# Optimization experiments

Measured on AMD Instinct MI355X. Metric: run time of the kernel, lower is better.

The kernel has to match this reference:

```python
import jax, jax.numpy as jnp
import numpy as np

B, S, D, H, F = 4, 1024, 2048, 16, 8192
HD = D // H  # head dim = 128
EPS = 1e-5


def layer_norm(x, w, b):
    mu = jnp.mean(x, axis=-1, keepdims=True)
    var = jnp.mean(jnp.square(x - mu), axis=-1, keepdims=True)
    return (x - mu) * jax.lax.rsqrt(var + EPS) * w + b


def setup_inputs() -> dict:
    key = jax.random.key(0)
    ks = jax.random.split(key, 12)
    s = 0.02  # realistic init scale for weights
    return {
        "x": jax.random.normal(ks[0], (B, S, D), jnp.float32),
        "attention_mask": jnp.zeros((B, 1, 1, S), jnp.float32),
        "wq": jax.random.normal(ks[1], (D, D), jnp.float32) * s,
        "bq": jax.random.normal(ks[2], (D,), jnp.float32) * s,
        "wk": jax.random.normal(ks[3], (D, D), jnp.float32) * s,
        "bk": jax.random.normal(ks[4], (D,), jnp.float32) * s,
        "wv": jax.random.normal(ks[5], (D, D), jnp.float32) * s,
        "bv": jax.random.normal(ks[6], (D,), jnp.float32) * s,
        "wo": jax.random.normal(ks[7], (D, D), jnp.float32) * s,
        "bo": jax.random.normal(ks[8], (D,), jnp.float32) * s,
        "ln1_w": jnp.ones((D,), jnp.float32),
        "ln1_b": jnp.zeros((D,), jnp.float32),
        "wi": jax.random.normal(ks[9], (F, D), jnp.float32) * s,
        "bi": jax.random.normal(ks[10], (F,), jnp.float32) * s,
        "wo2": jax.random.normal(ks[11], (D, F), jnp.float32) * s,
        "bo2": jnp.zeros((D,), jnp.float32),
        "ln2_w": jnp.ones((D,), jnp.float32),
        "ln2_b": jnp.zeros((D,), jnp.float32),
    }


def reference(x, attention_mask, wq, bq, wk, bk, wv, bv, wo, bo,
              ln1_w, ln1_b, wi, bi, wo2, bo2, ln2_w, ln2_b):
    # --- self attention ---
    q = (jnp.einsum('bsd,ed->bse', x, wq) + bq).reshape(B, S, H, HD).transpose(0, 2, 1, 3)
    k = (jnp.einsum('bsd,ed->bse', x, wk) + bk).reshape(B, S, H, HD).transpose(0, 2, 1, 3)
    v = (jnp.einsum('bsd,ed->bse', x, wv) + bv).reshape(B, S, H, HD).transpose(0, 2, 1, 3)
    scores = jnp.einsum('bhqd,bhkd->bhqk', q, k) / jnp.sqrt(jnp.float32(HD))
    scores = scores + attention_mask  # additive mask, broadcast over heads/query
    probs = jax.nn.softmax(scores, axis=-1)
    ctx = jnp.einsum('bhqk,bhkd->bhqd', probs, v)
    ctx = ctx.transpose(0, 2, 1, 3).reshape(B, S, D)
    # --- attention output: dense + bias + residual + LayerNorm ---
    attn_out = layer_norm(jnp.einsum('bsd,ed->bse', ctx, wo) + bo + x, ln1_w, ln1_b)
    # --- FFN: intermediate dense + bias, GELU, output dense + bias + residual + LN ---
    inter = jnp.einsum('bsd,fd->bsf', attn_out, wi) + bi
    h = jax.nn.gelu(inter, approximate=False)
    out = layer_norm(jnp.einsum('bsf,df->bsd', h, wo2) + bo2 + attn_out, ln2_w, ln2_b)
    return out
```

## Files before the change

### kernel.cpp

```cpp
#include <hip/hip_runtime.h>
#include <hip/hip_bf16.h>
#include <cstdint>
#include <cstddef>

typedef __attribute__((ext_vector_type(8))) short short8;
typedef __attribute__((ext_vector_type(4))) float f32x4;

#define DEV static __device__ __forceinline__

constexpr int kS = 1024, kD = 2048, kH = 16, kHD = 128, kF = 8192;
constexpr int kM = 4096;
constexpr float kEPS = 1e-5f;

constexpr size_t SZ_DD   = (size_t)kD * kD * 2;
constexpr size_t SZ_FD   = (size_t)kF * kD * 2;
constexpr size_t SZ_MD16 = (size_t)kM * kD * 2;
constexpr size_t SZ_MD32 = (size_t)kM * kD * 4;
constexpr size_t OFF_WQ  = 0;
constexpr size_t OFF_WK  = OFF_WQ + SZ_DD;
constexpr size_t OFF_WV  = OFF_WK + SZ_DD;
constexpr size_t OFF_WO  = OFF_WV + SZ_DD;
constexpr size_t OFF_WI  = OFF_WO + SZ_DD;
constexpr size_t OFF_WO2 = OFF_WI + SZ_FD;
constexpr size_t OFF_XB  = OFF_WO2 + SZ_FD;
constexpr size_t OFF_Q   = OFF_XB + SZ_MD16;
constexpr size_t OFF_K   = OFF_Q + SZ_MD16;
constexpr size_t OFF_V   = OFF_K + SZ_MD16;
constexpr size_t OFF_H   = OFF_XB;
constexpr size_t OFF_CTX = OFF_V + SZ_MD16;
constexpr size_t OFF_Y1  = OFF_CTX + SZ_MD16;
constexpr size_t OFF_A1B = OFF_Y1 + SZ_MD32;
constexpr size_t OFF_Y2  = OFF_A1B + SZ_MD16;
constexpr size_t WS_NEED = OFF_Y2 + SZ_MD32;

DEV void gload16(const void* g, void* l) {
  __builtin_amdgcn_global_load_lds(
      (const __attribute__((address_space(1))) unsigned int*)g,
      (__attribute__((address_space(3))) unsigned int*)l, 16, 0, 0);
}

__global__ void cvt_bf16(const float* __restrict__ in, __hip_bfloat16* __restrict__ out, int n4) {
  int stride = gridDim.x * blockDim.x;
  for (int i = blockIdx.x * blockDim.x + threadIdx.x; i < n4; i += stride) {
    float4 v = reinterpret_cast<const float4*>(in)[i];
    union { ushort4 u; __hip_bfloat16 h[4]; } o;
    o.h[0] = __float2bfloat16(v.x);
    o.h[1] = __float2bfloat16(v.y);
    o.h[2] = __float2bfloat16(v.z);
    o.h[3] = __float2bfloat16(v.w);
    reinterpret_cast<ushort4*>(out)[i] = o.u;
  }
}

template <int MODE>
__global__ __launch_bounds__(512, 2)
void gemm256(const __hip_bfloat16* __restrict__ A,
             const __hip_bfloat16* __restrict__ Bt,
             const float* __restrict__ bias,
             float* __restrict__ out0, float* __restrict__ out1,
             void* __restrict__ outb,
             int M, int N, int K, int kLen) {
  __shared__ __align__(16) char lds[131072];
  const int tid = threadIdx.x;
  const int lane = tid & 63, w = tid >> 6;
  const int wm = w >> 2, wn = w & 3;
  const int lg = lane >> 4, lr = lane & 15;
  const int gy = M >> 8, gx = N >> 8;
  const int nwg = gridDim.x, orig = blockIdx.x;
  const int l = (orig & 7) * (nwg >> 3) + (orig >> 3);
  const int tilesPer = gx * gy;
  const int spl = l / tilesPer;
  const int rem = l - spl * tilesPer;
  const int bx = rem / gy, by = rem - bx * gy;
  const int m0 = by * 256, n0 = bx * 256;
  const int k0 = spl * kLen;
  const int NT = kLen >> 6;

  const char* gs[8];
  #pragma unroll
  for (int h = 0; h < 4; ++h) {
    const __hip_bfloat16* src = (h < 2) ? A : Bt;
    const int r0 = ((h < 2) ? m0 : n0) + (h & 1) * 128;
    #pragma unroll
    for (int i = 0; i < 2; ++i) {
      int c = i * 512 + tid;
      int row = c >> 3, slot = c & 7;
      gs[h * 2 + i] =
          (const char*)(src + (size_t)(r0 + row) * K + k0 + (slot ^ (row & 7)) * 8);
    }
  }

#define STAGE(P, H, TOFF)                                                          \
  {                                                                                \
    char* dstb = lds + (((H) < 2) ? 0 : 65536) + (P) * 32768 + ((H) & 1) * 16384;  \
    gload16(gs[(H) * 2 + 0] + (TOFF) * 128, dstb + (0 * 512 + tid) * 16);          \
    gload16(gs[(H) * 2 + 1] + (TOFF) * 128, dstb + (1 * 512 + tid) * 16);          \
  }

  auto ldA = [&](int P, int qm, int mr, int kk) {
    int row = qm * 128 + wm * 64 + mr * 16 + lr;
    return *reinterpret_cast<const short8*>(
        lds + P * 32768 + row * 128 + (((kk * 4 + lg) ^ (row & 7)) * 16));
  };
  auto ldB = [&](int P, int qn, int nr, int kk) {
    int row = qn * 128 + wn * 32 + nr * 16 + lr;
    return *reinterpret_cast<const short8*>(
        lds + 65536 + P * 32768 + row * 128 + (((kk * 4 + lg) ^ (row & 7)) * 16));
  };

  f32x4 acc[4][4][2] = {};

#define MFMA_HALF(q, kk, B)                                                     \
  _Pragma("unroll")                                                             \
  for (int mi = 0; mi < 4; ++mi)                                                \
    _Pragma("unroll")                                                           \
    for (int ni = 0; ni < 2; ++ni)                                              \
      acc[q][mi][ni] = __builtin_amdgcn_mfma_f32_16x16x32_bf16(                 \
          av[kk][mi], B[kk][ni], acc[q][mi][ni], 0, 0, 0);

#define WAIT_LGKM(n)                                                            \
  asm volatile("s_waitcnt lgkmcnt(" #n ")" ::: "memory");                       \
  __builtin_amdgcn_sched_barrier(0);

#define TILE_BODY(P, PF)                                                        \
  {                                                                             \
               \
    asm volatile("s_waitcnt vmcnt(2)" ::: "memory");                            \
    __builtin_amdgcn_s_barrier();                                               \
         \
    _Pragma("unroll")                                                           \
    for (int i = 0; i < 4; ++i) av[0][i] = ldA(P, 0, i, 0);                     \
    _Pragma("unroll")                                                           \
    for (int i = 0; i < 2; ++i) b0[0][i] = ldB(P, 0, i, 0);                     \
    _Pragma("unroll")                                                           \
    for (int i = 0; i < 4; ++i) av[1][i] = ldA(P, 0, i, 1);                     \
    _Pragma("unroll")                                                           \
    for (int i = 0; i < 2; ++i) b0[1][i] = ldB(P, 0, i, 1);                     \
    _Pragma("unroll")                                                           \
    for (int i = 0; i < 2; ++i) b1[0][i] = ldB(P, 1, i, 0);                     \
    _Pragma("unroll")                                                           \
    for (int i = 0; i < 2; ++i) b1[1][i] = ldB(P, 1, i, 1);                     \
    if (PF) STAGE((P) ^ 1, 0, 1 + (P))                                          \
    WAIT_LGKM(10)                                                               \
    __builtin_amdgcn_s_setprio(1);                                              \
    MFMA_HALF(0, 0, b0)                                                         \
    WAIT_LGKM(4)                                                                \
    MFMA_HALF(0, 1, b0)                                                         \
    __builtin_amdgcn_s_setprio(0);                                              \
    if (PF) STAGE((P) ^ 1, 2, 1 + (P))                                          \
    WAIT_LGKM(2)                                                                \
    __builtin_amdgcn_s_setprio(1);                                              \
    MFMA_HALF(1, 0, b1)                                                         \
    WAIT_LGKM(0)                                                                \
    MFMA_HALF(1, 1, b1)                                                         \
    __builtin_amdgcn_s_setprio(0);                                              \
           \
    if (PF) { asm volatile("s_waitcnt vmcnt(4)" ::: "memory"); }                \
    else    { asm volatile("s_waitcnt vmcnt(0)" ::: "memory"); }                \
    __builtin_amdgcn_s_barrier();                                               \
    _Pragma("unroll")                                                           \
    for (int i = 0; i < 4; ++i) av[0][i] = ldA(P, 1, i, 0);                     \
    _Pragma("unroll")                                                           \
    for (int i = 0; i < 4; ++i) av[1][i] = ldA(P, 1, i, 1);                     \
    if (PF) STAGE((P) ^ 1, 3, 1 + (P))                                          \
    WAIT_LGKM(4)                                                                \
    __builtin_amdgcn_s_setprio(1);                                              \
    MFMA_HALF(2, 0, b1)                                                         \
    WAIT_LGKM(0)                                                                \
    MFMA_HALF(2, 1, b1)                                                         \
    __builtin_amdgcn_s_setprio(0);                                              \
    _Pragma("unroll")                                                           \
    for (int i = 0; i < 2; ++i) b0[0][i] = ldB(P, 0, i, 0);                     \
    _Pragma("unroll")                                                           \
    for (int i = 0; i < 2; ++i) b0[1][i] = ldB(P, 0, i, 1);                     \
    if (PF) STAGE((P) ^ 1, 1, 1 + (P))                                          \
    WAIT_LGKM(2)                                                                \
    __builtin_amdgcn_s_setprio(1);                                              \
    MFMA_HALF(3, 0, b0)                                                         \
    WAIT_LGKM(0)                                                                \
    MFMA_HALF(3, 1, b0)                                                         \
    __builtin_amdgcn_s_setprio(0);                                              \
  }

  STAGE(0, 0, 0) STAGE(0, 2, 0) STAGE(0, 3, 0) STAGE(0, 1, 0)

  for (int t2 = 0; t2 < NT; t2 += 2) {
    short8 av[2][4], b0[2][2], b1[2][2];
    TILE_BODY(0, true)
    TILE_BODY(1, (t2 + 2 < NT))
    #pragma unroll
    for (int j = 0; j < 8; ++j) gs[j] += 256;
  }
#undef TILE_BODY
#undef MFMA_HALF
#undef WAIT_LGKM
#undef STAGE

  #pragma unroll
  for (int q = 0; q < 4; ++q) {
    const int qm = (q >= 2) ? 1 : 0;
    const int qn = (q == 1 || q == 2) ? 1 : 0;
    #pragma unroll
    for (int ni = 0; ni < 2; ++ni) {
      int col = n0 + qn * 128 + wn * 32 + ni * 16 + lr;
      float bvv = 0.f;
      if constexpr (MODE != 3) bvv = bias[col];
      #pragma unroll
      for (int mi = 0; mi < 4; ++mi) {
        int row0 = m0 + qm * 128 + wm * 64 + mi * 16 + lg * 4;
        #pragma unroll
        for (int r = 0; r < 4; ++r) {
          int row = row0 + r;
          float val = acc[q][mi][ni][r] + bvv;
          if constexpr (MODE == 0) {
            int which = col >> 11;
            int d = col & 2047;
            int hh = d >> 7, hd = d & 127;
            int bb = row >> 10, ss = row & 1023;
            __hip_bfloat16* base = (__hip_bfloat16*)outb + (size_t)which * ((size_t)kM * kD);
            if (which < 2)
              base[(((size_t)(bb * kH + hh)) * kS + ss) * kHD + hd] = __float2bfloat16(val);
            else
              base[(((size_t)(bb * kH + hh)) * kHD + hd) * kS + ss] = __float2bfloat16(val);
          } else if constexpr (MODE == 2) {
            float g = 0.5f * val * (1.0f + erff(val * 0.70710678118654752f));
            ((__hip_bfloat16*)outb)[(size_t)row * N + col] = __float2bfloat16(g);
          } else {
            float* o = spl ? out1 : out0;
            o[(size_t)row * N + col] = val;
          }
        }
      }
    }
  }
}

__global__ __launch_bounds__(512, 4)
void attn_fwd(const __hip_bfloat16* __restrict__ q,
              const __hip_bfloat16* __restrict__ k,
              const __hip_bfloat16* __restrict__ vt,
              const float* __restrict__ mask,
              __hip_bfloat16* __restrict__ ctx) {
  __shared__ __align__(16) char Ks[2][64 * 256];
  __shared__ __align__(16) char Vt[2][128 * 128];
  __shared__ __align__(16) char Ps[8][2048];
  const int tid = threadIdx.x, lane = tid & 63, w = tid >> 6;
  const int lg = lane >> 4, lr = lane & 15;
  const int orig = blockIdx.x;
  const int l = (orig & 7) * 64 + (orig >> 3);
  const int qt = l & 7, bh = l >> 3;
  const int b = bh >> 4;

  short8 qf[4];
  {
    const __hip_bfloat16* qp =
        q + ((size_t)bh * kS + qt * 128 + w * 16 + lr) * kHD + lg * 8;
    #pragma unroll
    for (int kk = 0; kk < 4; ++kk) qf[kk] = *reinterpret_cast<const short8*>(qp + kk * 32);
  }

  auto stage = [&](int bufi, int t) {
    #pragma unroll
    for (int i = 0; i < 2; ++i) {
      int c = i * 512 + tid;
      int row = c >> 4, slot = c & 15;
      gload16(k + ((size_t)bh * kS + t * 64 + row) * kHD + (slot ^ (row & 15)) * 8,
              Ks[bufi] + c * 16);
    }
    #pragma unroll
    for (int i = 0; i < 2; ++i) {
      int c = i * 512 + tid;
      int row = c >> 3, slot = c & 7;
      gload16(vt + ((size_t)bh * kHD + row) * kS + t * 64 + (slot ^ (row & 7)) * 8,
              Vt[bufi] + c * 16);
    }
  };

  f32x4 o[8] = {};
  float mrun[4], lrun[4];
  #pragma unroll
  for (int r = 0; r < 4; ++r) { mrun[r] = -1e30f; lrun[r] = 0.f; }
  const float scale = 0.08838834764831845f;

  stage(0, 0);
  __syncthreads();

  int buf = 0;
  for (int t = 0; t < 16; ++t) {
    if (t + 1 < 16) stage(buf ^ 1, t + 1);

    f32x4 sacc[4] = {};
    #pragma unroll
    for (int j = 0; j < 4; ++j) {
      int key = j * 16 + lr;
      #pragma unroll
      for (int kk = 0; kk < 4; ++kk) {
        short8 bfrag = *reinterpret_cast<const short8*>(
            Ks[buf] + key * 256 + (((kk * 4 + lg) ^ (key & 15)) * 16));
        sacc[j] = __builtin_amdgcn_mfma_f32_16x16x32_bf16(qf[kk], bfrag, sacc[j], 0, 0, 0);
      }
    }
    float sarr[4][4];
    #pragma unroll
    for (int j = 0; j < 4; ++j) {
      float mv = mask[(size_t)b * kS + t * 64 + j * 16 + lr];
      #pragma unroll
      for (int r = 0; r < 4; ++r) sarr[j][r] = sacc[j][r] * scale + mv;
    }
    #pragma unroll
    for (int r = 0; r < 4; ++r) {
      float tm = fmaxf(fmaxf(sarr[0][r], sarr[1][r]), fmaxf(sarr[2][r], sarr[3][r]));
      #pragma unroll
      for (int d = 1; d < 16; d <<= 1) tm = fmaxf(tm, __shfl_xor(tm, d));
      float mnew = fmaxf(mrun[r], tm);
      float alpha = __expf(mrun[r] - mnew);
      mrun[r] = mnew;
      float rs = 0.f;
      #pragma unroll
      for (int j = 0; j < 4; ++j) {
        float p = __expf(sarr[j][r] - mnew);
        sarr[j][r] = p;
        rs += p;
      }
      #pragma unroll
      for (int d = 1; d < 16; d <<= 1) rs += __shfl_xor(rs, d);
      lrun[r] = lrun[r] * alpha + rs;
      #pragma unroll
      for (int n = 0; n < 8; ++n) o[n][r] *= alpha;
    }
    #pragma unroll
    for (int r = 0; r < 4; ++r) {
      int qr = lg * 4 + r;
      #pragma unroll
      for (int j = 0; j < 4; ++j)
        *reinterpret_cast<__hip_bfloat16*>(
            Ps[w] + ((qr * 128 + (j * 16 + lr) * 2) ^ ((qr & 7) << 4))) =
            __float2bfloat16(sarr[j][r]);
    }
    #pragma unroll
    for (int kk2 = 0; kk2 < 2; ++kk2) {
      short8 pa = *reinterpret_cast<const short8*>(
          Ps[w] + ((lr * 128 + kk2 * 64 + lg * 16) ^ ((lr & 7) << 4)));
      #pragma unroll
      for (int n = 0; n < 8; ++n) {
        int hd = n * 16 + lr;
        short8 vb = *reinterpret_cast<const short8*>(
            Vt[buf] + hd * 128 + (((kk2 * 4 + lg) ^ (hd & 7)) * 16));
        o[n] = __builtin_amdgcn_mfma_f32_16x16x32_bf16(pa, vb, o[n], 0, 0, 0);
      }
    }
    __syncthreads();
    buf ^= 1;
  }

  const int h = bh & 15;
  #pragma unroll
  for (int r = 0; r < 4; ++r) {
    float inv = 1.0f / lrun[r];
    int srow = qt * 128 + w * 16 + lg * 4 + r;
    __hip_bfloat16* cp = ctx + ((size_t)b * kS + srow) * kD + h * 128 + lr;
    #pragma unroll
    for (int n = 0; n < 8; ++n) cp[n * 16] = __float2bfloat16(o[n][r] * inv);
  }
}

template <bool WB16>
__global__ void ln_fuse(const float* __restrict__ p0, const float* __restrict__ p1,
                        const float* __restrict__ bias, const float* __restrict__ res,
                        const float* __restrict__ w, const float* __restrict__ b,
                        float* __restrict__ outf, __hip_bfloat16* __restrict__ outb) {
  const int row = blockIdx.x, tid = threadIdx.x;
  const size_t base = (size_t)row * kD;
  float v[8];
  #pragma unroll
  for (int i = 0; i < 2; ++i) {
    int c4 = tid * 2 + i;
    float4 a  = reinterpret_cast<const float4*>(p0 + base)[c4];
    float4 bb = reinterpret_cast<const float4*>(p1 + base)[c4];
    float4 rr = reinterpret_cast<const float4*>(res + base)[c4];
    float4 bs = reinterpret_cast<const float4*>(bias)[c4];
    v[i * 4 + 0] = a.x + bb.x + rr.x + bs.x;
    v[i * 4 + 1] = a.y + bb.y + rr.y + bs.y;
    v[i * 4 + 2] = a.z + bb.z + rr.z + bs.z;
    v[i * 4 + 3] = a.w + bb.w + rr.w + bs.w;
  }
  float s = 0.f;
  #pragma unroll
  for (int i = 0; i < 8; ++i) s += v[i];
  #pragma unroll
  for (int off = 32; off > 0; off >>= 1) s += __shfl_down(s, off);
  __shared__ float r1[4], r2[4];
  if ((tid & 63) == 0) r1[tid >> 6] = s;
  __syncthreads();
  float mean = (r1[0] + r1[1] + r1[2] + r1[3]) * (1.0f / kD);
  float qv = 0.f;
  #pragma unroll
  for (int i = 0; i < 8; ++i) { float d = v[i] - mean; qv += d * d; }
  #pragma unroll
  for (int off = 32; off > 0; off >>= 1) qv += __shfl_down(qv, off);
  if ((tid & 63) == 0) r2[tid >> 6] = qv;
  __syncthreads();
  float rstd = rsqrtf((r2[0] + r2[1] + r2[2] + r2[3]) * (1.0f / kD) + kEPS);
  #pragma unroll
  for (int i = 0; i < 8; ++i) {
    int col = tid * 8 + i;
    float ov = (v[i] - mean) * rstd * w[col] + b[col];
    outf[base + col] = ov;
    if constexpr (WB16) outb[base + col] = __float2bfloat16(ov);
  }
}

extern "C" void kernel_launch(void* const* d_in, const int* in_sizes, int n_in,
                              void* d_out, int out_size, void* d_ws, size_t ws_size,
                              hipStream_t stream) {
  (void)in_sizes; (void)n_in; (void)out_size;
  if (ws_size < WS_NEED) return;
  const float* x    = (const float*)d_in[0];
  const float* mask = (const float*)d_in[1];
  const float* wq   = (const float*)d_in[2];
  const float* bq   = (const float*)d_in[3];
  const float* wk   = (const float*)d_in[4];
  const float* bk   = (const float*)d_in[5];
  const float* wv   = (const float*)d_in[6];
  const float* bv   = (const float*)d_in[7];
  const float* wo   = (const float*)d_in[8];
  const float* bo   = (const float*)d_in[9];
  const float* l1w  = (const float*)d_in[10];
  const float* l1b  = (const float*)d_in[11];
  const float* wi   = (const float*)d_in[12];
  const float* bi   = (const float*)d_in[13];
  const float* wo2  = (const float*)d_in[14];
  const float* bo2  = (const float*)d_in[15];
  const float* l2w  = (const float*)d_in[16];
  const float* l2b  = (const float*)d_in[17];

  char* ws = (char*)d_ws;
  __hip_bfloat16* wqb  = (__hip_bfloat16*)(ws + OFF_WQ);
  __hip_bfloat16* wkb  = (__hip_bfloat16*)(ws + OFF_WK);
  __hip_bfloat16* wvb  = (__hip_bfloat16*)(ws + OFF_WV);
  __hip_bfloat16* wob  = (__hip_bfloat16*)(ws + OFF_WO);
  __hip_bfloat16* wib  = (__hip_bfloat16*)(ws + OFF_WI);
  __hip_bfloat16* wo2b = (__hip_bfloat16*)(ws + OFF_WO2);
  __hip_bfloat16* xb   = (__hip_bfloat16*)(ws + OFF_XB);
  __hip_bfloat16* qb   = (__hip_bfloat16*)(ws + OFF_Q);
  __hip_bfloat16* kb2  = (__hip_bfloat16*)(ws + OFF_K);
  __hip_bfloat16* vtb  = (__hip_bfloat16*)(ws + OFF_V);
  __hip_bfloat16* hb   = (__hip_bfloat16*)(ws + OFF_H);
  __hip_bfloat16* ctxb = (__hip_bfloat16*)(ws + OFF_CTX);
  __hip_bfloat16* a1b  = (__hip_bfloat16*)(ws + OFF_A1B);
  float* y1   = (float*)(ws + OFF_Y1);
  float* y2   = (float*)(ws + OFF_Y2);
  float* f2p  = (float*)(ws + OFF_WQ);
  float* bqkv = (float*)(ws + OFF_Y2);

  cvt_bf16<<<2048, 256, 0, stream>>>(x,   xb,   kM * kD / 4);
  cvt_bf16<<<1024, 256, 0, stream>>>(wq,  wqb,  kD * kD / 4);
  cvt_bf16<<<1024, 256, 0, stream>>>(wk,  wkb,  kD * kD / 4);
  cvt_bf16<<<1024, 256, 0, stream>>>(wv,  wvb,  kD * kD / 4);
  cvt_bf16<<<1024, 256, 0, stream>>>(wo,  wob,  kD * kD / 4);
  cvt_bf16<<<2048, 256, 0, stream>>>(wi,  wib,  kF * kD / 4);
  cvt_bf16<<<2048, 256, 0, stream>>>(wo2, wo2b, kF * kD / 4);
  hipMemcpyAsync(bqkv,          bq, kD * 4, hipMemcpyDeviceToDevice, stream);
  hipMemcpyAsync(bqkv + kD,     bk, kD * 4, hipMemcpyDeviceToDevice, stream);
  hipMemcpyAsync(bqkv + 2 * kD, bv, kD * 4, hipMemcpyDeviceToDevice, stream);

  dim3 blk(512);
  gemm256<0><<<dim3(384), blk, 0, stream>>>(
      xb, wqb, bqkv, nullptr, nullptr, qb, kM, 6144, kD, kD);
  attn_fwd<<<dim3(512), dim3(512), 0, stream>>>(qb, kb2, vtb, mask, ctxb);
  gemm256<3><<<dim3(256), blk, 0, stream>>>(
      ctxb, wob, nullptr, y1, y2, nullptr, kM, kD, kD, kD / 2);
  ln_fuse<true><<<kM, 256, 0, stream>>>(y1, y2, bo, x, l1w, l1b, y1, a1b);
  gemm256<2><<<dim3(512), blk, 0, stream>>>(
      a1b, wib, bi, nullptr, nullptr, hb, kM, kF, kD, kD);
  gemm256<3><<<dim3(256), blk, 0, stream>>>(
      hb, wo2b, nullptr, y2, f2p, nullptr, kM, kD, kF, kF / 2);
  ln_fuse<false><<<kM, 256, 0, stream>>>(y2, f2p, bo2, y1, l2w, l2b, (float*)d_out, nullptr);
}
```

Measured before the change: 675.3 us.

## Restructure GEMM tile loop into barrier-bracketed per-quadrant phases

```diff
diff --git a/kernel.cpp b/kernel.cpp
--- a/kernel.cpp
+++ b/kernel.cpp
@@ -110,24 +110,31 @@
 
   f32x4 acc[4][4][2] = {};
 
-#define MFMA_HALF(q, kk, B)                                                     \
+#define MFMA_QUAD(q, B)                                                         \
   _Pragma("unroll")                                                             \
-  for (int mi = 0; mi < 4; ++mi)                                                \
-    _Pragma("unroll")                                                           \
-    for (int ni = 0; ni < 2; ++ni)                                              \
-      acc[q][mi][ni] = __builtin_amdgcn_mfma_f32_16x16x32_bf16(                 \
-          av[kk][mi], B[kk][ni], acc[q][mi][ni], 0, 0, 0);
-
-#define WAIT_LGKM(n)                                                            \
-  asm volatile("s_waitcnt lgkmcnt(" #n ")" ::: "memory");                       \
-  __builtin_amdgcn_sched_barrier(0);
+  for (int kk = 0; kk < 2; ++kk)                                                \
+    _Pragma("unroll")                                                           \
+    for (int mi = 0; mi < 4; ++mi)                                              \
+      _Pragma("unroll")                                                         \
+      for (int ni = 0; ni < 2; ++ni)                                            \
+        acc[q][mi][ni] = __builtin_amdgcn_mfma_f32_16x16x32_bf16(               \
+            av[kk][mi], B[kk][ni], acc[q][mi][ni], 0, 0, 0);
+
+#define PHASE_CORE(Q, B, WAITSTMT)                                              \
+    __builtin_amdgcn_s_barrier();                                               \
+    asm volatile("s_waitcnt lgkmcnt(0)" ::: "memory");                          \
+    __builtin_amdgcn_sched_barrier(0);                                          \
+    __builtin_amdgcn_s_setprio(1);                                              \
+    MFMA_QUAD(Q, B)                                                             \
+    __builtin_amdgcn_s_setprio(0);                                              \
+    WAITSTMT                                                                    \
+    __builtin_amdgcn_s_barrier();
+
+#define VM(n) asm volatile("s_waitcnt vmcnt(" #n ")" ::: "memory");
 
 #define TILE_BODY(P, PF)                                                        \
   {                                                                             \
-               \
-    asm volatile("s_waitcnt vmcnt(2)" ::: "memory");                            \
-    __builtin_amdgcn_s_barrier();                                               \
-         \
+              \
     _Pragma("unroll")                                                           \
     for (int i = 0; i < 4; ++i) av[0][i] = ldA(P, 0, i, 0);                     \
     _Pragma("unroll")                                                           \
@@ -136,53 +143,34 @@
     for (int i = 0; i < 4; ++i) av[1][i] = ldA(P, 0, i, 1);                     \
     _Pragma("unroll")                                                           \
     for (int i = 0; i < 2; ++i) b0[1][i] = ldB(P, 0, i, 1);                     \
+    if (PF) STAGE((P) ^ 1, 0, 1 + (P))                                          \
+    if (PF) { PHASE_CORE(0, b0, VM(4)) } else { PHASE_CORE(0, b0, VM(2)) }      \
+      \
     _Pragma("unroll")                                                           \
     for (int i = 0; i < 2; ++i) b1[0][i] = ldB(P, 1, i, 0);                     \
     _Pragma("unroll")                                                           \
     for (int i = 0; i < 2; ++i) b1[1][i] = ldB(P, 1, i, 1);                     \
-    if (PF) STAGE((P) ^ 1, 0, 1 + (P))                                          \
-    WAIT_LGKM(10)                                                               \
-    __builtin_amdgcn_s_setprio(1);                                              \
-    MFMA_HALF(0, 0, b0)                                                         \
-    WAIT_LGKM(4)                                                                \
-    MFMA_HALF(0, 1, b0)                                                         \
-    __builtin_amdgcn_s_setprio(0);                                              \
     if (PF) STAGE((P) ^ 1, 2, 1 + (P))                                          \
-    WAIT_LGKM(2)                                                                \
-    __builtin_amdgcn_s_setprio(1);                                              \
-    MFMA_HALF(1, 0, b1)                                                         \
-    WAIT_LGKM(0)                                                                \
-    MFMA_HALF(1, 1, b1)                                                         \
-    __builtin_amdgcn_s_setprio(0);                                              \
-           \
-    if (PF) { asm volatile("s_waitcnt vmcnt(4)" ::: "memory"); }                \
-    else    { asm volatile("s_waitcnt vmcnt(0)" ::: "memory"); }                \
-    __builtin_amdgcn_s_barrier();                                               \
+    if (PF) { PHASE_CORE(1, b1, VM(4)) } else { PHASE_CORE(1, b1, VM(0)) }      \
+                         \
     _Pragma("unroll")                                                           \
     for (int i = 0; i < 4; ++i) av[0][i] = ldA(P, 1, i, 0);                     \
     _Pragma("unroll")                                                           \
     for (int i = 0; i < 4; ++i) av[1][i] = ldA(P, 1, i, 1);                     \
     if (PF) STAGE((P) ^ 1, 3, 1 + (P))                                          \
-    WAIT_LGKM(4)                                                                \
-    __builtin_amdgcn_s_setprio(1);                                              \
-    MFMA_HALF(2, 0, b1)                                                         \
-    WAIT_LGKM(0)                                                                \
-    MFMA_HALF(2, 1, b1)                                                         \
-    __builtin_amdgcn_s_setprio(0);                                              \
+    PHASE_CORE(2, b1, )                                                         \
+      \
     _Pragma("unroll")                                                           \
     for (int i = 0; i < 2; ++i) b0[0][i] = ldB(P, 0, i, 0);                     \
     _Pragma("unroll")                                                           \
     for (int i = 0; i < 2; ++i) b0[1][i] = ldB(P, 0, i, 1);                     \
     if (PF) STAGE((P) ^ 1, 1, 1 + (P))                                          \
-    WAIT_LGKM(2)                                                                \
-    __builtin_amdgcn_s_setprio(1);                                              \
-    MFMA_HALF(3, 0, b0)                                                         \
-    WAIT_LGKM(0)                                                                \
-    MFMA_HALF(3, 1, b0)                                                         \
-    __builtin_amdgcn_s_setprio(0);                                              \
+    if (PF) { PHASE_CORE(3, b0, VM(4)) } else { PHASE_CORE(3, b0, ) }           \
   }
 
   STAGE(0, 0, 0) STAGE(0, 2, 0) STAGE(0, 3, 0) STAGE(0, 1, 0)
+  VM(4)
+  __builtin_amdgcn_s_barrier();
 
   for (int t2 = 0; t2 < NT; t2 += 2) {
     short8 av[2][4], b0[2][2], b1[2][2];
@@ -192,8 +180,9 @@
     for (int j = 0; j < 8; ++j) gs[j] += 256;
   }
 #undef TILE_BODY
-#undef MFMA_HALF
-#undef WAIT_LGKM
+#undef PHASE_CORE
+#undef MFMA_QUAD
+#undef VM
 #undef STAGE
 
   #pragma unroll
```

After: 1.036 ms. 53.4% more time.
